# Kernel optimization log

Measured on AMD Instinct MI355X. Metric: run time of the kernel, lower is better.

The kernel has to match this reference:

```python
import jax, jax.numpy as jnp
import numpy as np

HEADS = 16
GROUPS = 4


def setup_inputs() -> dict:
    key = jax.random.key(0)
    k1, k2, k3, k4 = jax.random.split(key, 4)
    d_model = 2048
    d_kv = d_model * GROUPS // HEADS  # 512
    x = jax.random.normal(k1, (2, 2048, d_model), dtype=jnp.float32)
    Wq = jax.random.normal(k2, (d_model, d_model), dtype=jnp.float32) * (d_model ** -0.5)
    Wk = jax.random.normal(k3, (d_kv, d_model), dtype=jnp.float32) * (d_model ** -0.5)
    Wv = jax.random.normal(k4, (d_kv, d_model), dtype=jnp.float32) * (d_model ** -0.5)
    return {"x": x, "Wq": Wq, "Wk": Wk, "Wv": Wv}


def reference(x, Wq, Wk, Wv):
    b, t, c = x.shape
    hd = c // HEADS  # head dim
    h2g = HEADS // GROUPS  # query heads per kv group
    # projections (nn.Linear applies x @ W.T)
    q = (x @ Wq.T).reshape(b, t, HEADS, hd).transpose(0, 2, 1, 3)   # [b,H,t,hd]
    k = (x @ Wk.T).reshape(b, t, GROUPS, hd).transpose(0, 2, 1, 3)  # [b,G,t,hd]
    v = (x @ Wv.T).reshape(b, t, GROUPS, hd).transpose(0, 2, 1, 3)  # [b,G,t,hd]
    # GQA broadcast: group query heads by kv group
    qg = q.reshape(b, GROUPS, h2g, t, hd)                            # [b,G,h2g,t,hd]
    scores = jnp.einsum('bghqd,bgkd->bghqk', qg, k) * (hd ** -0.5)  # [b,G,h2g,t,t]
    causal = jnp.tril(jnp.ones((t, t), dtype=bool))
    scores = jnp.where(causal, scores, -jnp.inf)
    weights = jax.nn.softmax(scores, axis=-1)
    out = jnp.einsum('bghqk,bgkd->bghqd', weights, v)               # [b,G,h2g,t,hd]
    out = out.reshape(b, HEADS, t, hd).transpose(0, 2, 1, 3).reshape(b, t, c)
    return out
```

## Files before the change

kernel.cpp:

```cpp
#include <hip/hip_runtime.h>
#include <hip/hip_bf16.h>

typedef __bf16 bf16x8 __attribute__((ext_vector_type(8)));
typedef float f32x4 __attribute__((ext_vector_type(4)));

#define MFMA16(a,b,c) __builtin_amdgcn_mfma_f32_16x16x32_bf16(a,b,c,0,0,0)
#define GLL16(src, dst) __builtin_amdgcn_global_load_lds( \
    (const __attribute__((address_space(1))) unsigned int*)(src), \
    (__attribute__((address_space(3))) unsigned int*)(dst), 16, 0, 0)
#define WAIT_VM(n)  asm volatile("s_waitcnt vmcnt(" #n ")")
#define BAR() __builtin_amdgcn_s_barrier()

__device__ inline unsigned int pack_bf16(float a, float b) {
    unsigned short ua = __builtin_bit_cast(unsigned short, (__bf16)a);
    unsigned short ub = __builtin_bit_cast(unsigned short, (__bf16)b);
    return ((unsigned int)ub << 16) | ua;
}
__device__ inline short bf_s(float v) {
    __bf16 b = (__bf16)v;
    return __builtin_bit_cast(short, b);
}

__global__ void cvt_all(const float* __restrict__ x,  const float* __restrict__ wq,
                        const float* __restrict__ wk, const float* __restrict__ wv,
                        __bf16* __restrict__ xb, __bf16* __restrict__ wb) {
    long i = (long)(blockIdx.x * blockDim.x + threadIdx.x) * 8;
    const float* src; __bf16* dst;
    if (i < 8388608)       { src = x  + i;              dst = xb + i; }
    else if (i < 12582912) { src = wq + (i - 8388608);  dst = wb + (i - 8388608); }
    else if (i < 13631488) { src = wk + (i - 12582912); dst = wb + (i - 12582912 + 4194304); }
    else                   { src = wv + (i - 13631488); dst = wb + (i - 13631488 + 5242880); }
    float4 a = *(const float4*)src;
    float4 b = *(const float4*)(src + 4);
    bf16x8 r;
    r[0] = (__bf16)a.x; r[1] = (__bf16)a.y; r[2] = (__bf16)a.z; r[3] = (__bf16)a.w;
    r[4] = (__bf16)b.x; r[5] = (__bf16)b.y; r[6] = (__bf16)b.z; r[7] = (__bf16)b.w;
    *(bf16x8*)dst = r;
}

__global__ __launch_bounds__(512, 6) void gemm_qkv(const __bf16* __restrict__ A,
                                                   const __bf16* __restrict__ B,
                                                   __bf16* __restrict__ Qb,
                                                   __bf16* __restrict__ Kf,
                                                   __bf16* __restrict__ Vf,
                                                   float qscale) {
    const int K = 2048;
    __shared__ __bf16 As[2 * 4096];
    __shared__ __bf16 Bs[2 * 4096];

    int tid = threadIdx.x;
    int wave = tid >> 6, lane = tid & 63;
    int quad = lane >> 4, l16 = lane & 15;
    int wr = wave >> 1, wc = wave & 1;

    int tm = blockIdx.x & 31, tn = blockIdx.x >> 5;

    const __bf16* Abase = A + (size_t)tm * 128 * K + (size_t)l16 * K + quad * 8;
    const __bf16* Bbase = B + (size_t)tn * 128 * K + (size_t)l16 * K + quad * 8;

    f32x4 acc[2][4] = {};

    auto stage = [&](int kt, int buf) {
        GLL16(Abase + (size_t)wave * 16 * K + kt, As + buf * 4096 + wave * 512 + lane * 8);
        GLL16(Bbase + (size_t)wave * 16 * K + kt, Bs + buf * 4096 + wave * 512 + lane * 8);
    };

    const int nk = K >> 5;
    stage(0, 0);
    for (int it = 0; it < nk; ++it) {
        __syncthreads();
        if (it + 1 < nk) stage((it + 1) << 5, (it + 1) & 1);
        const __bf16* Ab = As + (it & 1) * 4096;
        const __bf16* Bb = Bs + (it & 1) * 4096;
        bf16x8 af[2], bfr[4];
#pragma unroll
        for (int m = 0; m < 2; ++m)
            af[m] = *(const bf16x8*)(Ab + (wr * 2 + m) * 512 + lane * 8);
#pragma unroll
        for (int n = 0; n < 4; ++n)
            bfr[n] = *(const bf16x8*)(Bb + (wc * 4 + n) * 512 + lane * 8);
#pragma unroll
        for (int m = 0; m < 2; ++m)
#pragma unroll
            for (int n = 0; n < 4; ++n)
                acc[m][n] = MFMA16(af[m], bfr[n], acc[m][n]);
    }

#pragma unroll
    for (int m = 0; m < 2; ++m) {
        int row0 = tm * 128 + wr * 32 + m * 16 + quad * 4;
        int bb = row0 >> 11, tok0 = row0 & 2047;
#pragma unroll
        for (int n = 0; n < 4; ++n) {
            int col = tn * 128 + wc * 64 + n * 16 + l16;
            if (tn < 16) {
#pragma unroll
                for (int r = 0; r < 4; ++r)
                    Qb[(size_t)(row0 + r) * 2048 + col] = (__bf16)(acc[m][n][r] * qscale);
            } else if (tn < 20) {
                int d_all = col - 2048;
                int g = d_all >> 7, dd = d_all & 127;
                int dt = dd >> 5, q4 = (dd >> 3) & 3, jj = dd & 7;
                int tb = tok0 >> 4, tl0 = tok0 & 15;
                __bf16* base = Kf + ((((size_t)(bb * 4 + g) * 128 + tb) * 4 + dt) * 512)
                               + (q4 * 16 + tl0) * 8 + jj;
#pragma unroll
                for (int r = 0; r < 4; ++r)
                    base[r * 8] = (__bf16)acc[m][n][r];
            } else {
                int d_all = col - 2560;
                int g = d_all >> 7, dd = d_all & 127;
                int nto = dd >> 4, dl = dd & 15;
                int ch = tok0 >> 6, kk = (tok0 >> 5) & 1;
                int q4v = (tok0 >> 3) & 3, jv0 = tok0 & 7;
                size_t off = ((((size_t)(bb * 4 + g) * 32 + ch) * 16) + nto * 2 + kk) * 512
                             + (q4v * 16 + dl) * 8 + jv0;
                short4 pk;
                pk.x = bf_s(acc[m][n][0]); pk.y = bf_s(acc[m][n][1]);
                pk.z = bf_s(acc[m][n][2]); pk.w = bf_s(acc[m][n][3]);
                *(short4*)(Vf + off) = pk;
            }
        }
    }
}

__global__ __launch_bounds__(256) void attn_mfma(const __bf16* __restrict__ Q,
                                                 const __bf16* __restrict__ Kf,
                                                 const __bf16* __restrict__ Vf,
                                                 float* __restrict__ O) {
    const int T = 2048, CM = 2048, HD = 128;
    __shared__ __bf16 Ks[2 * 8192];
    __shared__ __bf16 Vs[2 * 8192];
    __shared__ __bf16 Pl[8192];

    int tid = threadIdx.x;
    int wave = tid >> 6, lane = tid & 63;
    int quad = lane >> 4, l16 = lane & 15;

    int bg = blockIdx.x & 7;
    int slot = blockIdx.x >> 3;
    int qb = (slot < 32) ? (63 - slot) : (slot - 32);
    int b = bg >> 2, g = bg & 3;
    int h = g * 4 + wave;
    int q0 = qb * 32;

    bf16x8 qf[2][4];
    const __bf16* qbase = Q + (size_t)b * T * CM + (size_t)h * HD;
#pragma unroll
    for (int nt = 0; nt < 2; ++nt)
#pragma unroll
        for (int dt = 0; dt < 4; ++dt)
            qf[nt][dt] = *(const bf16x8*)(qbase + (size_t)(q0 + nt * 16 + l16) * CM
                                          + dt * 32 + quad * 8);

    const __bf16* kcb = Kf + (size_t)(b * 4 + g) * 262144;
    const __bf16* vcb = Vf + (size_t)(b * 4 + g) * 262144;

    float m_r[2] = {-1e30f, -1e30f}, l_r[2] = {0.f, 0.f};
    f32x4 o_acc[2][8] = {};
    __bf16* Pw = Pl + wave * 2048;

    auto stage_kv = [&](int ch, int buf) {
        const __bf16* kg = kcb + ch * 8192 + wave * 2048 + lane * 8;
        const __bf16* vg = vcb + ch * 8192 + wave * 2048 + lane * 8;
        __bf16* kl = Ks + buf * 8192 + wave * 2048 + lane * 8;
        __bf16* vl = Vs + buf * 8192 + wave * 2048 + lane * 8;
#pragma unroll
        for (int i = 0; i < 4; ++i) GLL16(kg + i * 512, kl + i * 512);
#pragma unroll
        for (int i = 0; i < 4; ++i) GLL16(vg + i * 512, vl + i * 512);
    };

    int nch = (qb >> 1) + 1;
    stage_kv(0, 0);
    for (int ch = 0; ch < nch; ++ch) {
        BAR();
        if (ch + 1 < nch) {
            stage_kv(ch + 1, (ch + 1) & 1);
            WAIT_VM(8);
        } else {
            WAIT_VM(0);
        }
        BAR();

        const __bf16* Kb = Ks + (ch & 1) * 8192;
        const __bf16* Vb = Vs + (ch & 1) * 8192;

        f32x4 st[2][4] = {};
        __builtin_amdgcn_s_setprio(1);
#pragma unroll
        for (int t = 0; t < 4; ++t)
#pragma unroll
            for (int dt = 0; dt < 4; ++dt) {
                bf16x8 kfv = *(const bf16x8*)(Kb + (t * 4 + dt) * 512 + lane * 8);
                st[0][t] = MFMA16(kfv, qf[0][dt], st[0][t]);
                st[1][t] = MFMA16(kfv, qf[1][dt], st[1][t]);
            }
        __builtin_amdgcn_s_setprio(0);

        bool diag = (ch == nch - 1);
        float alpha[2];
#pragma unroll
        for (int nt = 0; nt < 2; ++nt) {
            if (diag) {
                int qg = q0 + nt * 16 + l16;
#pragma unroll
                for (int t = 0; t < 4; ++t)
#pragma unroll
                    for (int r = 0; r < 4; ++r)
                        if (ch * 64 + t * 16 + quad * 4 + r > qg) st[nt][t][r] = -1e30f;
            }
            float cmax = -1e30f;
#pragma unroll
            for (int t = 0; t < 4; ++t)
                cmax = fmaxf(cmax, fmaxf(fmaxf(st[nt][t][0], st[nt][t][1]),
                                         fmaxf(st[nt][t][2], st[nt][t][3])));
            cmax = fmaxf(cmax, __shfl_xor(cmax, 16));
            cmax = fmaxf(cmax, __shfl_xor(cmax, 32));
            float mnew = fmaxf(m_r[nt], cmax);
            alpha[nt] = __expf(m_r[nt] - mnew);
            m_r[nt] = mnew;
            float ps = 0.f;
#pragma unroll
            for (int t = 0; t < 4; ++t) {
                float p0 = __expf(st[nt][t][0] - mnew);
                float p1 = __expf(st[nt][t][1] - mnew);
                float p2 = __expf(st[nt][t][2] - mnew);
                float p3 = __expf(st[nt][t][3] - mnew);
                ps += (p0 + p1) + (p2 + p3);
                int off = (nt * 2 + (t >> 1)) * 512 + ((t & 1) * 2 + (quad >> 1)) * 128
                          + l16 * 8 + (quad & 1) * 4;
                unsigned long long pk =
                    (unsigned long long)pack_bf16(p0, p1) |
                    ((unsigned long long)pack_bf16(p2, p3) << 32);
                *(unsigned long long*)(Pw + off) = pk;
            }
            ps += __shfl_xor(ps, 16);
            ps += __shfl_xor(ps, 32);
            l_r[nt] = l_r[nt] * alpha[nt] + ps;
        }

#pragma unroll
        for (int mt = 0; mt < 2; ++mt)
#pragma unroll
            for (int r = 0; r < 4; ++r) {
                float alr = __shfl(alpha[mt], quad * 4 + r);
#pragma unroll
                for (int nto = 0; nto < 8; ++nto)
                    o_acc[mt][nto][r] *= alr;
            }

        __builtin_amdgcn_s_setprio(1);
#pragma unroll
        for (int mt = 0; mt < 2; ++mt)
#pragma unroll
            for (int kk = 0; kk < 2; ++kk) {
                bf16x8 pf = *(const bf16x8*)(Pw + (mt * 2 + kk) * 512 + lane * 8);
#pragma unroll
                for (int nto = 0; nto < 8; ++nto) {
                    bf16x8 vf = *(const bf16x8*)(Vb + (nto * 2 + kk) * 512 + lane * 8);
                    o_acc[mt][nto] = MFMA16(pf, vf, o_acc[mt][nto]);
                }
            }
        __builtin_amdgcn_s_setprio(0);
    }

    float* obase = O + (size_t)b * T * CM + (size_t)h * HD;
#pragma unroll
    for (int mt = 0; mt < 2; ++mt) {
        float invl = 1.f / l_r[mt];
#pragma unroll
        for (int r = 0; r < 4; ++r) {
            float ir = __shfl(invl, quad * 4 + r);
            float* orow = obase + (size_t)(q0 + 16 * mt + quad * 4 + r) * CM;
#pragma unroll
            for (int nto = 0; nto < 8; ++nto)
                orow[nto * 16 + l16] = o_acc[mt][nto][r] * ir;
        }
    }
}

extern "C" void kernel_launch(void* const* d_in, const int* in_sizes, int n_in,
                              void* d_out, int out_size, void* d_ws, size_t ws_size,
                              hipStream_t stream) {
    const float* x  = (const float*)d_in[0];
    const float* Wq = (const float*)d_in[1];
    const float* Wk = (const float*)d_in[2];
    const float* Wv = (const float*)d_in[3];
    float* out = (float*)d_out;

    const float qscale = 0.08838834764831845f;

    __bf16* xb = (__bf16*)d_ws;
    __bf16* Wb = xb + 8388608;
    __bf16* Qb = Wb + 6291456;
    __bf16* Kfr = Qb + 8388608;
    __bf16* Vfr = Kfr + 2097152;

    cvt_all<<<7168, 256, 0, stream>>>(x, Wq, Wk, Wv, xb, Wb);
    gemm_qkv<<<768, 512, 0, stream>>>(xb, Wb, Qb, Kfr, Vfr, qscale);
    attn_mfma<<<512, 256, 0, stream>>>(Qb, Kfr, Vfr, out);
}
```

Baseline: 273.1 us.

## Pre-tile bf16 operands in conversion kernel for contiguous GEMM staging loads

```diff
diff --git a/kernel.cpp b/kernel.cpp
--- a/kernel.cpp
+++ b/kernel.cpp
@@ -21,21 +21,38 @@
     return __builtin_bit_cast(short, b);
 }
 
-__global__ void cvt_all(const float* __restrict__ x,  const float* __restrict__ wq,
-                        const float* __restrict__ wk, const float* __restrict__ wv,
-                        __bf16* __restrict__ xb, __bf16* __restrict__ wb) {
-    long i = (long)(blockIdx.x * blockDim.x + threadIdx.x) * 8;
-    const float* src; __bf16* dst;
-    if (i < 8388608)       { src = x  + i;              dst = xb + i; }
-    else if (i < 12582912) { src = wq + (i - 8388608);  dst = wb + (i - 8388608); }
-    else if (i < 13631488) { src = wk + (i - 12582912); dst = wb + (i - 12582912 + 4194304); }
-    else                   { src = wv + (i - 13631488); dst = wb + (i - 13631488 + 5242880); }
+__global__ __launch_bounds__(256) void cvt_all(const float* __restrict__ x,
+                                               const float* __restrict__ wq,
+                                               const float* __restrict__ wk,
+                                               const float* __restrict__ wv,
+                                               __bf16* __restrict__ xb,
+                                               __bf16* __restrict__ wb) {
+    int bid = blockIdx.x;
+    int rb = bid >> 4, ks = bid & 15;
+    int t = threadIdx.x;
+    int row = t & 15;
+    int k8 = ks * 16 + (t >> 4);
+    int k = k8 * 8;
+
+    const float* src;
+    __bf16* dptr;
+    size_t tin = (size_t)(k8 >> 2) * 512 + (size_t)(k8 & 3) * 128 + row * 8;
+    if (rb < 256) {
+        src  = x + (size_t)(rb * 16 + row) * 2048 + k;
+        dptr = xb + (size_t)rb * 32768 + tin;
+    } else {
+        int wr = (rb - 256) * 16 + row;
+        if (wr < 2048)      src = wq + (size_t)wr * 2048 + k;
+        else if (wr < 2560) src = wk + (size_t)(wr - 2048) * 2048 + k;
+        else                src = wv + (size_t)(wr - 2560) * 2048 + k;
+        dptr = wb + (size_t)(rb - 256) * 32768 + tin;
+    }
     float4 a = *(const float4*)src;
     float4 b = *(const float4*)(src + 4);
     bf16x8 r;
     r[0] = (__bf16)a.x; r[1] = (__bf16)a.y; r[2] = (__bf16)a.z; r[3] = (__bf16)a.w;
     r[4] = (__bf16)b.x; r[5] = (__bf16)b.y; r[6] = (__bf16)b.z; r[7] = (__bf16)b.w;
-    *(bf16x8*)dst = r;
+    *(bf16x8*)dptr = r;
 }
 
 __global__ __launch_bounds__(512, 6) void gemm_qkv(const __bf16* __restrict__ A,
@@ -44,7 +61,6 @@
                                                    __bf16* __restrict__ Kf,
                                                    __bf16* __restrict__ Vf,
                                                    float qscale) {
-    const int K = 2048;
     __shared__ __bf16 As[2 * 4096];
     __shared__ __bf16 Bs[2 * 4096];
 
@@ -55,21 +71,21 @@
 
     int tm = blockIdx.x & 31, tn = blockIdx.x >> 5;
 
-    const __bf16* Abase = A + (size_t)tm * 128 * K + (size_t)l16 * K + quad * 8;
-    const __bf16* Bbase = B + (size_t)tn * 128 * K + (size_t)l16 * K + quad * 8;
+    const __bf16* Atile = A + (size_t)(tm * 8 + wave) * 32768 + lane * 8;
+    const __bf16* Btile = B + (size_t)(tn * 8 + wave) * 32768 + lane * 8;
 
     f32x4 acc[2][4] = {};
 
-    auto stage = [&](int kt, int buf) {
-        GLL16(Abase + (size_t)wave * 16 * K + kt, As + buf * 4096 + wave * 512 + lane * 8);
-        GLL16(Bbase + (size_t)wave * 16 * K + kt, Bs + buf * 4096 + wave * 512 + lane * 8);
+    auto stage = [&](int kb, int buf) {
+        GLL16(Atile + (size_t)kb * 512, As + buf * 4096 + wave * 512 + lane * 8);
+        GLL16(Btile + (size_t)kb * 512, Bs + buf * 4096 + wave * 512 + lane * 8);
     };
 
-    const int nk = K >> 5;
+    const int nk = 64;
     stage(0, 0);
     for (int it = 0; it < nk; ++it) {
         __syncthreads();
-        if (it + 1 < nk) stage((it + 1) << 5, (it + 1) & 1);
+        if (it + 1 < nk) stage(it + 1, (it + 1) & 1);
         const __bf16* Ab = As + (it & 1) * 4096;
         const __bf16* Bb = Bs + (it & 1) * 4096;
         bf16x8 af[2], bfr[4];
```

Result: faster. 231.2 us (-15.3%).
